# Performance work log

Measured on AMD Instinct MI355X. Metric: run time of the kernel, lower is better.

The kernel has to match this reference:

```python
import jax, jax.numpy as jnp
import numpy as np

B, S, H, NH = 2, 2048, 1024, 16
HD = H // NH
EPS = 1e-6

def rotate_half(x):
    x1, x2 = jnp.split(x, 2, axis=-1)
    return jnp.concatenate([-x2, x1], axis=-1)

def setup_inputs() -> dict:
    key = jax.random.key(0)
    ks = jax.random.split(key, 4)
    x = jax.random.normal(ks[0], (B, S, H), dtype=jnp.float32)
    # rotary angles
    inv_freq = 1.0 / (10000.0 ** (np.arange(0, HD, 2, dtype=np.float32) / HD))
    t = np.arange(S, dtype=np.float32)
    freqs = np.einsum('s,d->sd', t, inv_freq)
    emb = np.concatenate([freqs, freqs], axis=-1)  # [S, HD]
    cos = jnp.broadcast_to(jnp.cos(emb)[None], (B, S, HD)).astype(jnp.float32)
    sin = jnp.broadcast_to(jnp.sin(emb)[None], (B, S, HD)).astype(jnp.float32)
    attn_mask = jnp.broadcast_to(jnp.tril(jnp.ones((S, S), jnp.float32))[None], (B, S, S))
    W_uvqk = jax.random.normal(ks[1], (4 * H, H), dtype=jnp.float32) * (1.0 / np.sqrt(H))
    b_uvqk = jnp.zeros((4 * H,), jnp.float32)
    gate_w = jnp.ones((H,), jnp.float32)
    W_out = jax.random.normal(ks[2], (H, H), dtype=jnp.float32) * (1.0 / np.sqrt(H))
    b_out = jnp.zeros((H,), jnp.float32)
    return {"x": x, "cos": cos, "sin": sin, "attn_mask": attn_mask,
            "W_uvqk": W_uvqk, "b_uvqk": b_uvqk, "gate_w": gate_w,
            "W_out": W_out, "b_out": b_out}

def reference(x, cos, sin, attn_mask, W_uvqk, b_uvqk, gate_w, W_out, b_out):
    b, s, h = x.shape
    residual = x
    uvqk = jnp.einsum('bsh,oh->bso', x, W_uvqk) + b_uvqk
    u, v, q, k = jnp.split(uvqk, 4, axis=-1)
    u = jax.nn.silu(u)
    q = q.reshape(b, s, NH, HD)
    k = k.reshape(b, s, NH, HD)
    v = v.reshape(b, s, NH, HD)
    c = cos[:, :, None, :]  # [B,S,1,HD] broadcasts over heads
    sn = sin[:, :, None, :]
    q = q * c + rotate_half(q) * sn
    k = k * c + rotate_half(k) * sn
    # [B,NH,S,S] raw scores -> silu (no softmax) -> mask -> AV
    scores = jnp.einsum('bqnd,bknd->bnqk', q, k) / np.sqrt(HD).astype(np.float32)
    attn = jax.nn.silu(scores) * attn_mask[:, None, :, :]
    attn_out = jnp.einsum('bnqk,bknd->bqnd', attn, v).reshape(b, s, h)
    # RMSNorm (fp32) gating
    ao32 = attn_out.astype(jnp.float32)
    var = jnp.mean(ao32 * ao32, axis=-1, keepdims=True)
    normed = (gate_w * (ao32 * jax.lax.rsqrt(var + EPS))).astype(x.dtype)
    gated = normed * u
    out = jnp.einsum('bsh,oh->bso', gated, W_out) + b_out
    return residual + out
```

## Files before the change

kernel.cpp:

```cpp
#include <hip/hip_runtime.h>

typedef __attribute__((ext_vector_type(4))) float f32x4;
typedef __attribute__((ext_vector_type(8))) short short8;

static __device__ __forceinline__ unsigned short f2bf(float f) {
    union { float f; unsigned int u; } v; v.f = f;
    unsigned int r = v.u + 0x7FFFu + ((v.u >> 16) & 1u);
    return (unsigned short)(r >> 16);
}

static __device__ __forceinline__ float bf2f(unsigned short h) {
    union { unsigned int u; float f; } v; v.u = ((unsigned int)h) << 16;
    return v.f;
}

static __device__ __forceinline__ unsigned int cvt_pk_bf16(float lo, float hi) {
    unsigned int r;
    asm("v_cvt_pk_bf16_f32 %0, %1, %2" : "=v"(r) : "v"(lo), "v"(hi));
    return r;
}

static __device__ __forceinline__ void gload16(const void* g, void* l) {
    __builtin_amdgcn_global_load_lds(
        (const __attribute__((address_space(1))) unsigned int*)g,
        (__attribute__((address_space(3))) unsigned int*)l, 16, 0, 0);
}

__global__ __launch_bounds__(256) void k_convert(
    const float* __restrict__ x, const float* __restrict__ wu, const float* __restrict__ wo,
    unsigned short* __restrict__ xb, unsigned short* __restrict__ wub, unsigned short* __restrict__ wob)
{
    int i = blockIdx.x * 256 + threadIdx.x;
    const float* src; unsigned short* dst; int off;
    if (i < 1048576)       { src = x;  dst = xb;  off = i; }
    else if (i < 2097152)  { src = wu; dst = wub; off = i - 1048576; }
    else                   { src = wo; dst = wob; off = i - 2097152; }
    float4 v = reinterpret_cast<const float4*>(src)[off];
    ushort4 o;
    o.x = f2bf(v.x); o.y = f2bf(v.y); o.z = f2bf(v.z); o.w = f2bf(v.w);
    reinterpret_cast<ushort4*>(dst)[off] = o;
}

template<int MODE>
__global__ __launch_bounds__(256) void k_gemm(
    const unsigned short* __restrict__ A, const unsigned short* __restrict__ Bmat,
    const float* __restrict__ bias,
    unsigned short* __restrict__ u_out, unsigned short* __restrict__ q_out,
    unsigned short* __restrict__ k_out, unsigned short* __restrict__ vt_out,
    const float* __restrict__ cosp, const float* __restrict__ sinp,
    const float* __restrict__ resid, float* __restrict__ out)
{
    const int K = 1024;
    constexpr int BM = (MODE == 0) ? 128 : 64;
    constexpr int MT = BM / 32;
    constexpr int ACH = BM * 8 / 256;
    __shared__ __align__(16) unsigned short AsBs[BM * 64 + 128 * 64];
    unsigned short* As = AsBs;
    unsigned short* Bs = AsBs + BM * 64;
    int tid = threadIdx.x;
    int lane = tid & 63, wid = tid >> 6;
    int lo = lane & 15, q4 = lane >> 4;
    int x7 = lo & 7;
    int wr = wid >> 1, wc = wid & 1;
    int bn = blockIdx.x, bm = blockIdx.y;
    const unsigned short* Abase = A + (size_t)bm * BM * K;
    const unsigned short* Bbase = Bmat + (size_t)bn * 128 * K;

    f32x4 acc[MT][4] = {};
    for (int kt = 0; kt < K / 64; ++kt) {
#pragma unroll
        for (int j = 0; j < ACH; ++j) {
            int ch = tid + j * 256;
            int r = ch >> 3, p = ch & 7;
            gload16(Abase + (size_t)r * K + kt * 64 + (p ^ (r & 7)) * 8, As + ch * 8);
        }
#pragma unroll
        for (int j = 0; j < 4; ++j) {
            int ch = tid + j * 256;
            int r = ch >> 3, p = ch & 7;
            gload16(Bbase + (size_t)r * K + kt * 64 + (p ^ (r & 7)) * 8, Bs + ch * 8);
        }
        __syncthreads();
#pragma unroll
        for (int kc = 0; kc < 2; ++kc) {
            short8 af[MT], bfr[4];
#pragma unroll
            for (int t = 0; t < MT; ++t)
                af[t] = *(const short8*)&As[(wr * (BM / 2) + t * 16 + lo) * 64 + (((kc * 4 + q4) ^ x7) * 8)];
#pragma unroll
            for (int t = 0; t < 4; ++t)
                bfr[t] = *(const short8*)&Bs[(wc * 64 + t * 16 + lo) * 64 + (((kc * 4 + q4) ^ x7) * 8)];
#pragma unroll
            for (int mt = 0; mt < MT; ++mt)
#pragma unroll
                for (int nt = 0; nt < 4; ++nt)
                    acc[mt][nt] = __builtin_amdgcn_mfma_f32_16x16x32_bf16(af[mt], bfr[nt], acc[mt][nt], 0, 0, 0);
        }
        __syncthreads();
    }

    int rowb = bm * BM + wr * (BM / 2);
    int colb = bn * 128 + wc * 64;
    if (MODE == 0) {
        int region = colb >> 10;
        if (region == 1) {
            unsigned short* T = AsBs;
#pragma unroll
            for (int mt = 0; mt < MT; ++mt)
#pragma unroll
                for (int nt = 0; nt < 4; ++nt) {
                    float bcol = bias[colb + nt * 16 + lo];
                    uint2 w;
                    w.x = cvt_pk_bf16(acc[mt][nt][0] + bcol, acc[mt][nt][1] + bcol);
                    w.y = cvt_pk_bf16(acc[mt][nt][2] + bcol, acc[mt][nt][3] + bcol);
                    int c_local = wc * 64 + nt * 16 + lo;
                    int schunk = wr * 8 + mt * 2 + (q4 >> 1);
                    *(uint2*)((char*)T + c_local * 256 + ((schunk ^ (c_local & 15)) * 16) + (q4 & 1) * 8) = w;
                }
            __syncthreads();
            int c_row = tid >> 1;
            int bchunk = (tid & 1) * 8;
            int c_global = (bn - 8) * 128 + c_row;
            int head = c_global >> 6, d = c_global & 63;
            int batch = (bm * 128) >> 11;
            unsigned short* vrow = vt_out + ((size_t)(batch * 16 + head) * 64 + d) * 2048;
#pragma unroll
            for (int i = 0; i < 8; ++i) {
                int chunk = bchunk + i;
                uint4 v = *(const uint4*)((const char*)T + c_row * 256 + ((chunk ^ (c_row & 15)) * 16));
                int s = (bm * 128 + chunk * 8) & 2047;
                *(uint4*)&vrow[s] = v;
            }
        } else {
#pragma unroll
            for (int mt = 0; mt < MT; ++mt) {
#pragma unroll
                for (int r = 0; r < 4; ++r) {
                    int rg = rowb + mt * 16 + q4 * 4 + r;
                    int b = rg >> 11, s = rg & 2047;
                    float vals[4];
#pragma unroll
                    for (int nt = 0; nt < 4; ++nt)
                        vals[nt] = acc[mt][nt][r] + bias[colb + nt * 16 + lo];
                    if (region == 0) {
#pragma unroll
                        for (int nt = 0; nt < 4; ++nt) {
                            float vv = vals[nt];
                            u_out[(size_t)rg * 1024 + colb + nt * 16 + lo] = f2bf(vv / (1.f + __expf(-vv)));
                        }
                    } else {
                        const float* cb = cosp + (size_t)(b * 2048 + s) * 64;
                        const float* sb = sinp + (size_t)(b * 2048 + s) * 64;
                        float o[4];
#pragma unroll
                        for (int nt = 0; nt < 4; ++nt) {
                            int hd = nt * 16 + lo;
                            float partner = (nt < 2) ? -vals[nt + 2] : vals[nt - 2];
                            o[nt] = vals[nt] * cb[hd] + partner * sb[hd];
                        }
                        int c0 = colb - ((region == 2) ? 2048 : 3072);
                        unsigned short* dst = (region == 2) ? q_out : k_out;
#pragma unroll
                        for (int nt = 0; nt < 4; ++nt) {
                            int c = c0 + nt * 16 + lo;
                            int head = c >> 6, d = c & 63;
                            dst[((size_t)(b * 16 + head) * 2048 + s) * 64 + d] = f2bf(o[nt]);
                        }
                    }
                }
            }
        }
    } else {
#pragma unroll
        for (int mt = 0; mt < MT; ++mt)
#pragma unroll
            for (int r = 0; r < 4; ++r) {
                int rg = rowb + mt * 16 + q4 * 4 + r;
#pragma unroll
                for (int nt = 0; nt < 4; ++nt) {
                    int c = colb + nt * 16 + lo;
                    out[(size_t)rg * 1024 + c] = acc[mt][nt][r] + bias[c] + resid[(size_t)rg * 1024 + c];
                }
            }
    }
}

__global__ __launch_bounds__(256) void k_attn(
    const unsigned short* __restrict__ Q, const unsigned short* __restrict__ Kg,
    const unsigned short* __restrict__ Vt_g, float* __restrict__ AO0, float* __restrict__ AO1)
{
    __shared__ __align__(16) unsigned short Ksb[2][64 * 64];
    __shared__ __align__(16) unsigned short Vsb[2][64 * 64];
    __shared__ __align__(16) unsigned short Ps[4 * 2048];
    int tid = threadIdx.x;
    int lane = tid & 63, wid = tid >> 6;
    int lo = lane & 15, q4 = lane >> 4;
    int bid = blockIdx.x;
    int bh = bid & 31;
    int s  = bid >> 5;
    int b = bh >> 4, head = bh & 15;

    const unsigned short* Qb = Q    + (size_t)bh * 2048 * 64;
    const unsigned short* Kb = Kg   + (size_t)bh * 2048 * 64;
    const unsigned short* Vb = Vt_g + (size_t)bh * 64 * 2048;
    unsigned short* Pw = Ps + wid * 2048;

    int i0 = wid * 128 + lane;
    int i1 = wid * 128 + 64 + lane;
    int c_0 = i0 & 7, r_0 = i0 >> 3;
    int c_1 = i1 & 7, r_1 = i1 >> 3;
    int cs0 = c_0 ^ (r_0 & 7), cs1 = c_1 ^ (r_1 & 7);
    size_t kOff0 = (size_t)r_0 * 64 + cs0 * 8,  kOff1 = (size_t)r_1 * 64 + cs1 * 8;
    size_t vOff0 = (size_t)r_0 * 2048 + cs0 * 8, vOff1 = (size_t)r_1 * 2048 + cs1 * 8;

    int x7 = lo & 7, qr_rel = q4 >> 1;
    char* pw0 = (char*)Pw + (lo)      * 128 + (q4 & 1) * 8;
    char* pw1 = (char*)Pw + (lo + 16) * 128 + (q4 & 1) * 8;
    int swz[8];
#pragma unroll
    for (int cc = 0; cc < 8; ++cc) swz[cc] = (cc ^ x7) * 16;
    const short8* prd[2][2];
#pragma unroll
    for (int kc = 0; kc < 2; ++kc) {
        prd[0][kc] = (const short8*)&Pw[(lo) * 64      + (((kc * 4 + q4) ^ x7) * 8)];
        prd[1][kc] = (const short8*)&Pw[(16 + lo) * 64 + (((kc * 4 + q4) ^ x7) * 8)];
    }

    auto stage = [&](int bb, int kt) {
        gload16(Kb + (size_t)kt * 4096 + kOff0, &Ksb[bb][i0 * 8]);
        gload16(Kb + (size_t)kt * 4096 + kOff1, &Ksb[bb][i1 * 8]);
        gload16(Vb + (size_t)kt * 64 + vOff0, &Vsb[bb][i0 * 8]);
        gload16(Vb + (size_t)kt * 64 + vOff1, &Vsb[bb][i1 * 8]);
    };

    int J = s;
    int q0w = J * 128 + wid * 32;
    short8 qf[2][2];
#pragma unroll
    for (int qt = 0; qt < 2; ++qt)
#pragma unroll
        for (int kc = 0; kc < 2; ++kc)
            qf[qt][kc] = *(const short8*)(Qb + (size_t)(q0w + qt * 16 + lo) * 64 + kc * 32 + q4 * 8);

    f32x4 oacc[2][4] = {};
    stage(0, 0);
    __syncthreads();
    int buf = 0;

    for (int t = 0; t < 17; ++t) {
        int kt = (t <= s) ? t : (t + 15 - 2 * s);
        if (t < 16) {
            int tn = t + 1;
            int ktn = (tn <= s) ? tn : (tn + 15 - 2 * s);
            stage(buf ^ 1, ktn);
        }
        if (64 * kt <= q0w + 31) {
            f32x4 sacc[4][2] = {};
#pragma unroll
            for (int kc = 0; kc < 2; ++kc)
#pragma unroll
                for (int kt4 = 0; kt4 < 4; ++kt4) {
                    short8 kf = *(const short8*)&Ksb[buf][(kt4 * 16 + lo) * 64 + (((kc * 4 + q4) ^ x7) * 8)];
#pragma unroll
                    for (int qt = 0; qt < 2; ++qt)
                        sacc[kt4][qt] = __builtin_amdgcn_mfma_f32_16x16x32_bf16(kf, qf[qt][kc], sacc[kt4][qt], 0, 0, 0);
                }
            bool needMask = (64 * kt + 63 > q0w);
#pragma unroll
            for (int kt4 = 0; kt4 < 4; ++kt4)
#pragma unroll
                for (int qt = 0; qt < 2; ++qt) {
                    int qc = qt * 16 + lo;
                    float p[4];
#pragma unroll
                    for (int rr = 0; rr < 4; ++rr) {
                        float S = sacc[kt4][qt][rr];
                        float e = __builtin_amdgcn_exp2f(S * -0.180336880f);
                        float pv = S * 0.125f * __builtin_amdgcn_rcpf(1.f + e);
                        if (needMask) {
                            int ky = kt * 64 + kt4 * 16 + q4 * 4 + rr;
                            if (ky > q0w + qc) pv = 0.f;
                        }
                        p[rr] = pv;
                    }
                    uint2 w;
                    w.x = cvt_pk_bf16(p[0], p[1]);
                    w.y = cvt_pk_bf16(p[2], p[3]);
                    *(uint2*)(((qt == 0) ? pw0 : pw1) + swz[kt4 * 2 + qr_rel]) = w;
                }
#pragma unroll
            for (int kc = 0; kc < 2; ++kc) {
                short8 pf0 = *prd[0][kc];
                short8 pf1 = *prd[1][kc];
#pragma unroll
                for (int nt = 0; nt < 4; ++nt) {
                    short8 vf = *(const short8*)&Vsb[buf][(nt * 16 + lo) * 64 + (((kc * 4 + q4) ^ x7) * 8)];
                    oacc[0][nt] = __builtin_amdgcn_mfma_f32_16x16x32_bf16(pf0, vf, oacc[0][nt], 0, 0, 0);
                    oacc[1][nt] = __builtin_amdgcn_mfma_f32_16x16x32_bf16(pf1, vf, oacc[1][nt], 0, 0, 0);
                }
            }
        }
        if (t == s) {
            float* aoLane = AO0 + ((size_t)(b * 2048 + q0w + q4 * 4)) * 1024 + head * 64 + lo;
#pragma unroll
            for (int qt = 0; qt < 2; ++qt)
#pragma unroll
                for (int nt = 0; nt < 4; ++nt)
#pragma unroll
                    for (int rr = 0; rr < 4; ++rr) {
                        aoLane[(qt * 16 + rr) * 1024 + nt * 16] = oacc[qt][nt][rr];
                        oacc[qt][nt][rr] = 0.f;
                    }
            J = 15 - s;
            q0w = J * 128 + wid * 32;
#pragma unroll
            for (int qt = 0; qt < 2; ++qt)
#pragma unroll
                for (int kc = 0; kc < 2; ++kc)
                    qf[qt][kc] = *(const short8*)(Qb + (size_t)(q0w + qt * 16 + lo) * 64 + kc * 32 + q4 * 8);
        }
        __syncthreads();
        buf ^= 1;
    }
    float* aoLane = AO1 + ((size_t)(b * 2048 + q0w + q4 * 4)) * 1024 + head * 64 + lo;
#pragma unroll
    for (int qt = 0; qt < 2; ++qt)
#pragma unroll
        for (int nt = 0; nt < 4; ++nt)
#pragma unroll
            for (int rr = 0; rr < 4; ++rr)
                aoLane[(qt * 16 + rr) * 1024 + nt * 16] = oacc[qt][nt][rr];
}

__global__ __launch_bounds__(256) void k_rmsgate(
    const float* __restrict__ AO0, const float* __restrict__ AO1, const unsigned short* __restrict__ U,
    const float* __restrict__ gw, unsigned short* __restrict__ G)
{
    __shared__ float red[4];
    int row = blockIdx.x, t = threadIdx.x;
    float4 a0 = *(const float4*)&AO0[(size_t)row * 1024 + t * 4];
    float4 a1 = *(const float4*)&AO1[(size_t)row * 1024 + t * 4];
    float4 a;
    a.x = a0.x + a1.x; a.y = a0.y + a1.y; a.z = a0.z + a1.z; a.w = a0.w + a1.w;
    float ss = a.x * a.x + a.y * a.y + a.z * a.z + a.w * a.w;
#pragma unroll
    for (int off = 32; off; off >>= 1) ss += __shfl_down(ss, off);
    int wid = t >> 6, lane = t & 63;
    if (lane == 0) red[wid] = ss;
    __syncthreads();
    float tot = red[0] + red[1] + red[2] + red[3];
    float rs = rsqrtf(tot * (1.f / 1024.f) + 1e-6f);
    float4 g = *(const float4*)&gw[t * 4];
    ushort4 uv = *(const ushort4*)&U[(size_t)row * 1024 + t * 4];
    ushort4 o;
    o.x = f2bf(g.x * a.x * rs * bf2f(uv.x));
    o.y = f2bf(g.y * a.y * rs * bf2f(uv.y));
    o.z = f2bf(g.z * a.z * rs * bf2f(uv.z));
    o.w = f2bf(g.w * a.w * rs * bf2f(uv.w));
    *(ushort4*)&G[(size_t)row * 1024 + t * 4] = o;
}

extern "C" void kernel_launch(void* const* d_in, const int* in_sizes, int n_in,
                              void* d_out, int out_size, void* d_ws, size_t ws_size,
                              hipStream_t stream) {
    const float* x      = (const float*)d_in[0];
    const float* cosp   = (const float*)d_in[1];
    const float* sinp   = (const float*)d_in[2];
    const float* b_uvqk = (const float*)d_in[5];
    const float* gate_w = (const float*)d_in[6];
    const float* b_out  = (const float*)d_in[8];
    float* out = (float*)d_out;

    char* ws = (char*)d_ws;
    unsigned short* xb  = (unsigned short*)(ws);
    unsigned short* wub = (unsigned short*)(ws + 8388608);
    unsigned short* wob = (unsigned short*)(ws + 16777216);
    unsigned short* ub  = (unsigned short*)(ws + 18874368);
    unsigned short* qb  = (unsigned short*)(ws + 35651584);
    unsigned short* kb  = (unsigned short*)(ws + 44040192);
    unsigned short* vtb = (unsigned short*)(ws + 52428800);
    float*          aob = (float*)(ws + 60817408);
    unsigned short* gb  = (unsigned short*)(ws + 77594624);
    float*          ao1 = (float*)(ws);

    k_convert<<<9216, 256, 0, stream>>>((const float*)d_in[0], (const float*)d_in[4],
                                        (const float*)d_in[7], xb, wub, wob);
    k_gemm<0><<<dim3(32, 32), 256, 0, stream>>>(xb, wub, b_uvqk, ub, qb, kb, vtb,
                                                cosp, sinp, nullptr, nullptr);
    k_attn<<<512, 256, 0, stream>>>(qb, kb, vtb, aob, ao1);
    k_rmsgate<<<4096, 256, 0, stream>>>(aob, ao1, ub, gate_w, gb);
    k_gemm<1><<<dim3(8, 64), 256, 0, stream>>>(gb, wob, b_out, nullptr, nullptr, nullptr, nullptr,
                                               nullptr, nullptr, x, out);
}
```

Measured before the change: 134.7 us.

## Double-buffer GEMM LDS tiles with async global-to-LDS prefetch

The GEMM main loop now uses two LDS buffers and issues the global_load_lds prefetch for tile k+1 before computing on tile k. It waits with explicit vmcnt counts so only the previous stage's loads must land, and uses raw s_barrier instead of __syncthreads. This aims to hide global load latency behind MFMA work, at the cost of twice the LDS footprint, which may reduce occupancy. The hand-tuned vmcnt values must match the per-stage load counts exactly.

```diff
diff --git a/kernel.cpp b/kernel.cpp
--- a/kernel.cpp
+++ b/kernel.cpp
@@ -24,6 +24,12 @@
     __builtin_amdgcn_global_load_lds(
         (const __attribute__((address_space(1))) unsigned int*)g,
         (__attribute__((address_space(3))) unsigned int*)l, 16, 0, 0);
+}
+
+static __device__ __forceinline__ void block_sync_raw() {
+    asm volatile("" ::: "memory");
+    __builtin_amdgcn_s_barrier();
+    asm volatile("" ::: "memory");
 }
 
 __global__ __launch_bounds__(256) void k_convert(
@@ -51,12 +57,13 @@
     const float* __restrict__ resid, float* __restrict__ out)
 {
     const int K = 1024;
+    constexpr int NT = 16;
     constexpr int BM = (MODE == 0) ? 128 : 64;
     constexpr int MT = BM / 32;
-    constexpr int ACH = BM * 8 / 256;
-    __shared__ __align__(16) unsigned short AsBs[BM * 64 + 128 * 64];
-    unsigned short* As = AsBs;
-    unsigned short* Bs = AsBs + BM * 64;
+    constexpr int ACH = BM / 32;
+    constexpr int ASZ = BM * 64;
+    constexpr int BSZ = 128 * 64;
+    __shared__ __align__(16) unsigned short S[2 * (ASZ + BSZ)];
     int tid = threadIdx.x;
     int lane = tid & 63, wid = tid >> 6;
     int lo = lane & 15, q4 = lane >> 4;
@@ -66,8 +73,9 @@
     const unsigned short* Abase = A + (size_t)bm * BM * K;
     const unsigned short* Bbase = Bmat + (size_t)bn * 128 * K;
 
-    f32x4 acc[MT][4] = {};
-    for (int kt = 0; kt < K / 64; ++kt) {
+    auto stage = [&](int bb, int kt) {
+        unsigned short* As = S + bb * (ASZ + BSZ);
+        unsigned short* Bs = As + ASZ;
 #pragma unroll
         for (int j = 0; j < ACH; ++j) {
             int ch = tid + j * 256;
@@ -80,7 +88,22 @@
             int r = ch >> 3, p = ch & 7;
             gload16(Bbase + (size_t)r * K + kt * 64 + (p ^ (r & 7)) * 8, Bs + ch * 8);
         }
-        __syncthreads();
+    };
+
+    f32x4 acc[MT][4] = {};
+    stage(0, 0);
+    int buf = 0;
+    for (int kt = 0; kt < NT; ++kt) {
+        if (kt + 1 < NT) {
+            stage(buf ^ 1, kt + 1);
+            if constexpr (MODE == 0) { asm volatile("s_waitcnt vmcnt(8)" ::: "memory"); }
+            else                     { asm volatile("s_waitcnt vmcnt(6)" ::: "memory"); }
+        } else {
+            asm volatile("s_waitcnt vmcnt(0)" ::: "memory");
+        }
+        block_sync_raw();
+        const unsigned short* As = S + buf * (ASZ + BSZ);
+        const unsigned short* Bs = As + ASZ;
 #pragma unroll
         for (int kc = 0; kc < 2; ++kc) {
             short8 af[MT], bfr[4];
@@ -96,7 +119,8 @@
                 for (int nt = 0; nt < 4; ++nt)
                     acc[mt][nt] = __builtin_amdgcn_mfma_f32_16x16x32_bf16(af[mt], bfr[nt], acc[mt][nt], 0, 0, 0);
         }
-        __syncthreads();
+        block_sync_raw();
+        buf ^= 1;
     }
 
     int rowb = bm * BM + wr * (BM / 2);
@@ -104,7 +128,7 @@
     if (MODE == 0) {
         int region = colb >> 10;
         if (region == 1) {
-            unsigned short* T = AsBs;
+            unsigned short* T = S;
 #pragma unroll
             for (int mt = 0; mt < MT; ++mt)
 #pragma unroll
```

Result: faster. 127.8 us (-5.1%).
